# Kernel tuning notes

Measured on AMD Instinct MI355X. Metric: run time of the kernel, lower is better.

The kernel has to match this reference:

```python
import jax, jax.numpy as jnp
import numpy as np

G, N, H, L = 128, 32, 128, 6  # graphs, nodes/graph, hidden, conv layers


def _ln(x, g, b, eps=1e-5):
    m = jnp.mean(x, axis=-1, keepdims=True)
    v = jnp.var(x, axis=-1, keepdims=True)
    return (x - m) * jax.lax.rsqrt(v + eps) * g + b


def setup_inputs() -> dict:
    key = jax.random.key(0)
    ks = jax.random.split(key, 16)
    s = float(H) ** -0.5
    return {
        "x_idx": jax.random.randint(ks[0], (G * N,), 0, 32, dtype=jnp.int32),
        "ea_idx": jax.random.randint(ks[1], (G, N, N), 0, 16, dtype=jnp.int32),
        "tf_idx": jax.random.randint(ks[2], (G, N, N), 0, 16, dtype=jnp.int32),
        "adj": jax.random.randint(ks[3], (G, N, N), 0, 2, dtype=jnp.int32),
        "emb_x": 0.2 * jax.random.normal(ks[4], (32, H), dtype=jnp.float32),
        "emb_ea": 0.2 * jax.random.normal(ks[5], (16, H), dtype=jnp.float32),
        "emb_tf": 0.2 * jax.random.normal(ks[6], (16, H), dtype=jnp.float32),
        "W0": s * jax.random.normal(ks[7], (H, H), dtype=jnp.float32),
        "b0": jnp.zeros((H,), jnp.float32),
        "W1": s * jax.random.normal(ks[8], (H, H), dtype=jnp.float32),
        "b1": jnp.zeros((H,), jnp.float32),
        "Wc": s * jax.random.normal(ks[9], (L, H, H), dtype=jnp.float32),
        "bc": jnp.zeros((L, H), jnp.float32),
        "gc": jnp.ones((L, H), jnp.float32),
        "cc": jnp.zeros((L, H), jnp.float32),
        "Wp": s * jax.random.normal(ks[10], (H, H), dtype=jnp.float32),
        "bp": jnp.zeros((H,), jnp.float32),
        "gp": jnp.ones((H,), jnp.float32),
        "cp": jnp.zeros((H,), jnp.float32),
        "Wq1": s * jax.random.normal(ks[11], (H, H), dtype=jnp.float32),
        "bq1": jnp.zeros((H,), jnp.float32),
        "gq1": jnp.ones((H,), jnp.float32),
        "cq1": jnp.zeros((H,), jnp.float32),
        "Wq2": s * jax.random.normal(ks[12], (H, 1), dtype=jnp.float32),
        "bq2": jnp.zeros((1,), jnp.float32),
    }


def reference(x_idx, ea_idx, tf_idx, adj, emb_x, emb_ea, emb_tf,
              W0, b0, W1, b1, Wc, bc, gc, cc, Wp, bp, gp, cp,
              Wq1, bq1, gq1, cq1, Wq2, bq2):
    # InputEncoderSp: embedding lookups
    x = emb_x[x_idx]                                           # [G*N, H]
    Aval = emb_ea[ea_idx] * adj[..., None].astype(emb_ea.dtype)  # [G,N,N,H] masked edge emb
    # tupleinit: unpooling_fromdense1dim gathers lin(x) to tuple dims 0/1
    x0 = (x @ W0 + b0).reshape(G, N, H)
    x1 = (x @ W1 + b1).reshape(G, N, H)
    X = x0[:, :, None, :] * x1[:, None, :, :] * emb_tf[tf_idx]  # [G,N,N,H]
    for l in range(L):
        tX = jax.nn.relu(_ln(X @ Wc[l] + bc[l], gc[l], cc[l]))
        msg = jnp.einsum('gikh,gkjh->gijh', tX, Aval)          # sum_k tX[i,k]*A[k,j]
        X = X + msg
    # OpPoolingSubg2D('S','mean'): pool tuple dim 1 -> node features
    xs = jnp.mean(X, axis=2).reshape(G * N, H)                 # [G*N, H]
    xs = jax.nn.relu(_ln(xs @ Wp + bp, gp, cp))                # poolmlp
    hg = jnp.sum(xs.reshape(G, N, H), axis=1)                  # node->graph sum pool [G,H]
    # pred_lin: 2-layer MLP, tailact=False
    h = jax.nn.relu(_ln(hg @ Wq1 + bq1, gq1, cq1))
    return h @ Wq2 + bq2                                       # [G, num_tasks=1]
```

## Files before the change

kernel.cpp:

```cpp
#include <hip/hip_runtime.h>

#define G 128
#define N 32
#define H 128
#define L 6

typedef _Float16 half8 __attribute__((ext_vector_type(8)));
typedef float f32x4 __attribute__((ext_vector_type(4)));

union H8 { unsigned u[4]; half8 v; };

__device__ inline unsigned short f16_bits(_Float16 h) {
  union { _Float16 f; unsigned short u; } c; c.f = h; return c.u;
}

__device__ inline unsigned packf16(float x) {
  _Float16 hi = (_Float16)x;
  _Float16 lo = (_Float16)(x - (float)hi);
  return (unsigned)f16_bits(hi) | ((unsigned)f16_bits(lo) << 16);
}

__global__ __launch_bounds__(256) void k_emb_mm(
    const float* __restrict__ emb_x,
    const float* __restrict__ W0, const float* __restrict__ b0, float* __restrict__ P0,
    const float* __restrict__ W1, const float* __restrict__ b1, float* __restrict__ P1) {
  const float* W = blockIdx.x ? W1 : W0;
  const float* b = blockIdx.x ? b1 : b0;
  float*       P = blockIdx.x ? P1 : P0;
  __shared__ float embs_t[128 * 32];
  int tid = threadIdx.x;
  {
    int i = tid & 31, k0 = (tid >> 5) * 16;
    const float* src = emb_x + i * 128 + k0;
#pragma unroll
    for (int m = 0; m < 16; m++) embs_t[(k0 + m) * 32 + i] = src[m];
  }
  __syncthreads();
  int i  = tid >> 3;
  int h0 = (tid & 7) * 16;
  float acc[16];
#pragma unroll
  for (int hh = 0; hh < 16; hh++) acc[hh] = b[h0 + hh];
  for (int k = 0; k < 128; k++) {
    float a = embs_t[k * 32 + i];
    const float4* wr = (const float4*)(W + k * 128 + h0);
    float4 w0 = wr[0], w1 = wr[1], w2 = wr[2], w3 = wr[3];
    acc[0]  += a * w0.x; acc[1]  += a * w0.y; acc[2]  += a * w0.z; acc[3]  += a * w0.w;
    acc[4]  += a * w1.x; acc[5]  += a * w1.y; acc[6]  += a * w1.z; acc[7]  += a * w1.w;
    acc[8]  += a * w2.x; acc[9]  += a * w2.y; acc[10] += a * w2.z; acc[11] += a * w2.w;
    acc[12] += a * w3.x; acc[13] += a * w3.y; acc[14] += a * w3.z; acc[15] += a * w3.w;
  }
  float4* dst = (float4*)(P + i * 128 + h0);
  dst[0] = make_float4(acc[0], acc[1], acc[2], acc[3]);
  dst[1] = make_float4(acc[4], acc[5], acc[6], acc[7]);
  dst[2] = make_float4(acc[8], acc[9], acc[10], acc[11]);
  dst[3] = make_float4(acc[12], acc[13], acc[14], acc[15]);
}

__global__ __launch_bounds__(256) void k_buildX(
    const int* __restrict__ x_idx, const int* __restrict__ tf_idx,
    const float* __restrict__ P0, const float* __restrict__ P1,
    const float* __restrict__ emb_tf, float* __restrict__ Xp) {
  int g = blockIdx.x, tid = threadIdx.x;
  __shared__ float x0t[128 * 32];
  __shared__ float x1t[128 * 32];
  __shared__ float etf[128 * 16];
  __shared__ int   tfs[1024];
  {
    int i = tid & 31, h0 = (tid >> 5) * 16;
    int r = x_idx[g * 32 + i];
    const float* s0 = P0 + r * 128 + h0;
    const float* s1 = P1 + r * 128 + h0;
#pragma unroll
    for (int m = 0; m < 16; m++) {
      x0t[(h0 + m) * 32 + i] = s0[m];
      x1t[(h0 + m) * 32 + i] = s1[m];
    }
  }
  {
    int t = tid & 15, h0 = (tid >> 4) * 8;
    const float* s = emb_tf + t * 128 + h0;
#pragma unroll
    for (int m = 0; m < 8; m++) etf[(h0 + m) * 16 + t] = s[m];
  }
  ((int4*)tfs)[tid] = ((const int4*)(tf_idx + (size_t)g * 1024))[tid];
  __syncthreads();
  int i = tid >> 3, j0 = (tid & 7) * 4;
  int t0 = tfs[i * 32 + j0 + 0], t1 = tfs[i * 32 + j0 + 1];
  int t2 = tfs[i * 32 + j0 + 2], t3 = tfs[i * 32 + j0 + 3];
  float* outg = Xp + ((size_t)g << 17);
  for (int h = 0; h < 128; h++) {
    float a = x0t[h * 32 + i];
    const float* x1r = x1t + h * 32;
    const float* er  = etf + h * 16;
    float4 v;
    v.x = a * x1r[j0 + 0] * er[t0];
    v.y = a * x1r[j0 + 1] * er[t1];
    v.z = a * x1r[j0 + 2] * er[t2];
    v.w = a * x1r[j0 + 3] * er[t3];
    *(float4*)(outg + h * 1024 + tid * 4) = v;
  }
}

__global__ __launch_bounds__(256, 2) void k_conv_mlp(
    const float* __restrict__ Xp, const float* __restrict__ W,
    const float* __restrict__ bcl, const float* __restrict__ gcl,
    const float* __restrict__ ccl, float* __restrict__ tXp) {
  int g = blockIdx.x >> 2, qb = blockIdx.x & 3;
  int tid = threadIdx.x;
  __shared__ unsigned Xs[256 * 32];
  __shared__ unsigned Ws[128 * 32];
  int lane = tid & 63, wv = tid >> 6;
  int x = lane & 15, quad = lane >> 4;

  f32x4 acc[4][8];
#pragma unroll
  for (int hh = 0; hh < 8; hh++) {
    float4 b4 = *(const float4*)(bcl + hh * 16 + quad * 4);
    f32x4 bi; bi[0] = b4.x; bi[1] = b4.y; bi[2] = b4.z; bi[3] = b4.w;
#pragma unroll
    for (int pt = 0; pt < 4; pt++) acc[pt][hh] = bi;
  }

  const float* Xg = Xp + ((size_t)g << 17) + qb * 256;

  for (int c = 0; c < 4; c++) {
    __syncthreads();
    {
      unsigned pk[8][4];
#pragma unroll
      for (int m = 0; m < 8; m++) {
        float4 v = *(const float4*)(Xg + (size_t)(c * 32 + wv * 8 + m) * 1024 + lane * 4);
        pk[m][0] = packf16(v.x); pk[m][1] = packf16(v.y);
        pk[m][2] = packf16(v.z); pk[m][3] = packf16(v.w);
      }
#pragma unroll
      for (int r = 0; r < 4; r++) {
        int p = 4 * lane + r;
        int sw = (p >> 2) & 7;
#pragma unroll
        for (int B2 = 0; B2 < 2; B2++) {
          int B = wv * 2 + B2;
          uint4 q4;
          q4.x = pk[B2 * 4 + 0][r]; q4.y = pk[B2 * 4 + 1][r];
          q4.z = pk[B2 * 4 + 2][r]; q4.w = pk[B2 * 4 + 3][r];
          *(uint4*)&Xs[p * 32 + ((B ^ sw) << 2)] = q4;
        }
      }
    }
    {
#pragma unroll
      for (int m = 0; m < 4; m++) {
        int f4 = m * 64 + lane;
        int kk = wv * 8 + (f4 >> 5);
        int h4 = (f4 & 31) * 4;
        float4 v = *(const float4*)(W + (size_t)(c * 32 + kk) * 128 + h4);
        int Bk = kk >> 2, km = kk & 3;
#pragma unroll
        for (int j = 0; j < 4; j++) {
          float vv = j == 0 ? v.x : (j == 1 ? v.y : (j == 2 ? v.z : v.w));
          int h = h4 + j;
          Ws[h * 32 + (((Bk ^ ((h >> 2) & 7)) << 2) + km)] = packf16(vv);
        }
      }
    }
    __syncthreads();
    H8 bh[4], bl[4];
#pragma unroll
    for (int pt = 0; pt < 4; pt++) {
      int p = wv * 64 + pt * 16 + x;
      int sw = (p >> 2) & 7;
#pragma unroll
      for (int n = 0; n < 4; n++) {
        int k = quad * 8 + n * 2;
        uint2 d = *(const uint2*)&Xs[p * 32 + (((k >> 2) ^ sw) << 2) + (k & 3)];
        bh[pt].u[n] = __builtin_amdgcn_perm(d.y, d.x, 0x05040100u);
        bl[pt].u[n] = __builtin_amdgcn_perm(d.y, d.x, 0x07060302u);
      }
    }
#pragma unroll
    for (int hh = 0; hh < 8; hh++) {
      H8 ah, al;
      int hrow = hh * 16 + x;
      int sw = (hrow >> 2) & 7;
#pragma unroll
      for (int n = 0; n < 4; n++) {
        int k = quad * 8 + n * 2;
        uint2 d = *(const uint2*)&Ws[hrow * 32 + (((k >> 2) ^ sw) << 2) + (k & 3)];
        ah.u[n] = __builtin_amdgcn_perm(d.y, d.x, 0x05040100u);
        al.u[n] = __builtin_amdgcn_perm(d.y, d.x, 0x07060302u);
      }
#pragma unroll
      for (int pt = 0; pt < 4; pt++) {
        acc[pt][hh] = __builtin_amdgcn_mfma_f32_16x16x32_f16(ah.v, bh[pt].v, acc[pt][hh], 0, 0, 0);
        acc[pt][hh] = __builtin_amdgcn_mfma_f32_16x16x32_f16(ah.v, bl[pt].v, acc[pt][hh], 0, 0, 0);
        acc[pt][hh] = __builtin_amdgcn_mfma_f32_16x16x32_f16(al.v, bh[pt].v, acc[pt][hh], 0, 0, 0);
      }
    }
  }

  float gm[4], gr[4];
#pragma unroll
  for (int pt = 0; pt < 4; pt++) {
    float s = 0.f;
#pragma unroll
    for (int hh = 0; hh < 8; hh++)
#pragma unroll
      for (int r = 0; r < 4; r++) s += acc[pt][hh][r];
    s += __shfl_xor(s, 16);
    s += __shfl_xor(s, 32);
    float m = s * (1.f / 128.f);
    float qv = 0.f;
#pragma unroll
    for (int hh = 0; hh < 8; hh++)
#pragma unroll
      for (int r = 0; r < 4; r++) { float d = acc[pt][hh][r] - m; qv += d * d; }
    qv += __shfl_xor(qv, 16);
    qv += __shfl_xor(qv, 32);
    gm[pt] = m;
    gr[pt] = rsqrtf(qv * (1.f / 128.f) + 1e-5f);
  }
  int pbase = qb * 256 + wv * 64;
#pragma unroll
  for (int hh = 0; hh < 8; hh++) {
    float4 g4 = *(const float4*)(gcl + hh * 16 + quad * 4);
    float4 c4 = *(const float4*)(ccl + hh * 16 + quad * 4);
    float ga[4] = {g4.x, g4.y, g4.z, g4.w};
    float ca[4] = {c4.x, c4.y, c4.z, c4.w};
#pragma unroll
    for (int r = 0; r < 4; r++) {
      int h = hh * 16 + quad * 4 + r;
      float* dst = tXp + (((size_t)(g * 128 + h)) << 10) + pbase + x;
#pragma unroll
      for (int pt = 0; pt < 4; pt++) {
        float v = (acc[pt][hh][r] - gm[pt]) * gr[pt] * ga[r] + ca[r];
        dst[pt * 16] = fmaxf(v, 0.f);
      }
    }
  }
}

__global__ __launch_bounds__(256, 4) void k_conv_msg(
    const float* __restrict__ tXp, const int* __restrict__ ea_idx,
    const int* __restrict__ adj, const float* __restrict__ emb_ea,
    float* __restrict__ Xp) {
  int g  = blockIdx.x >> 4;
  int hb = (blockIdx.x & 15) * 8;
  int tid = threadIdx.x, wv = tid >> 6, lane = tid & 63;
  __shared__ unsigned char c8[1024];
  __shared__ float eacs[8][20];
  __shared__ __align__(16) float tXs[4][32 * 36];
  __shared__ __align__(16) float As[4][32 * 36];
  {
    int4 ev = ((const int4*)(ea_idx + (size_t)g * 1024))[tid];
    int4 av = ((const int4*)(adj   + (size_t)g * 1024))[tid];
    uchar4 c;
    c.x = av.x ? (unsigned char)ev.x : (unsigned char)16;
    c.y = av.y ? (unsigned char)ev.y : (unsigned char)16;
    c.z = av.z ? (unsigned char)ev.z : (unsigned char)16;
    c.w = av.w ? (unsigned char)ev.w : (unsigned char)16;
    ((uchar4*)c8)[tid] = c;
  }
  if (tid < 128) {
    int hh = tid >> 4, e = tid & 15;
    eacs[hh][e] = emb_ea[e * 128 + hb + hh];
  }
  if (tid >= 128 && tid < 136) eacs[tid - 128][16] = 0.f;
  __syncthreads();
  int i0 = (lane >> 3) * 4, j0 = (lane & 7) * 4;
  float* tw = tXs[wv];
  float* aw = As[wv];
#pragma unroll 1
  for (int pl = 0; pl < 2; pl++) {
    int hh = wv * 2 + pl;
    int h  = hb + hh;
    const float4* tp = (const float4*)(tXp + (((size_t)(g * 128 + h)) << 10));
#pragma unroll
    for (int m = 0; m < 4; m++) {
      int f = lane + 64 * m;
      float4 v = tp[f];
      *(float4*)&tw[(f >> 3) * 36 + (f & 7) * 4] = v;
    }
#pragma unroll
    for (int m = 0; m < 4; m++) {
      int qd = lane + 64 * m;
      uchar4 cc = ((const uchar4*)c8)[qd];
      float4 a;
      a.x = eacs[hh][cc.x]; a.y = eacs[hh][cc.y];
      a.z = eacs[hh][cc.z]; a.w = eacs[hh][cc.w];
      *(float4*)&aw[(qd >> 3) * 36 + (qd & 7) * 4] = a;
    }
    float4 a0 = {0, 0, 0, 0}, a1 = a0, a2 = a0, a3 = a0;
#pragma unroll
    for (int kb = 0; kb < 8; kb++) {
      int k4 = kb * 4;
      float4 t0 = *(const float4*)&tw[(i0 + 0) * 36 + k4];
      float4 t1 = *(const float4*)&tw[(i0 + 1) * 36 + k4];
      float4 t2 = *(const float4*)&tw[(i0 + 2) * 36 + k4];
      float4 t3 = *(const float4*)&tw[(i0 + 3) * 36 + k4];
      float4 b0 = *(const float4*)&aw[(k4 + 0) * 36 + j0];
      float4 b1 = *(const float4*)&aw[(k4 + 1) * 36 + j0];
      float4 b2 = *(const float4*)&aw[(k4 + 2) * 36 + j0];
      float4 b3 = *(const float4*)&aw[(k4 + 3) * 36 + j0];
      a0.x += t0.x * b0.x; a0.y += t0.x * b0.y; a0.z += t0.x * b0.z; a0.w += t0.x * b0.w;
      a0.x += t0.y * b1.x; a0.y += t0.y * b1.y; a0.z += t0.y * b1.z; a0.w += t0.y * b1.w;
      a0.x += t0.z * b2.x; a0.y += t0.z * b2.y; a0.z += t0.z * b2.z; a0.w += t0.z * b2.w;
      a0.x += t0.w * b3.x; a0.y += t0.w * b3.y; a0.z += t0.w * b3.z; a0.w += t0.w * b3.w;
      a1.x += t1.x * b0.x; a1.y += t1.x * b0.y; a1.z += t1.x * b0.z; a1.w += t1.x * b0.w;
      a1.x += t1.y * b1.x; a1.y += t1.y * b1.y; a1.z += t1.y * b1.z; a1.w += t1.y * b1.w;
      a1.x += t1.z * b2.x; a1.y += t1.z * b2.y; a1.z += t1.z * b2.z; a1.w += t1.z * b2.w;
      a1.x += t1.w * b3.x; a1.y += t1.w * b3.y; a1.z += t1.w * b3.z; a1.w += t1.w * b3.w;
      a2.x += t2.x * b0.x; a2.y += t2.x * b0.y; a2.z += t2.x * b0.z; a2.w += t2.x * b0.w;
      a2.x += t2.y * b1.x; a2.y += t2.y * b1.y; a2.z += t2.y * b1.z; a2.w += t2.y * b1.w;
      a2.x += t2.z * b2.x; a2.y += t2.z * b2.y; a2.z += t2.z * b2.z; a2.w += t2.z * b2.w;
      a2.x += t2.w * b3.x; a2.y += t2.w * b3.y; a2.z += t2.w * b3.z; a2.w += t2.w * b3.w;
      a3.x += t3.x * b0.x; a3.y += t3.x * b0.y; a3.z += t3.x * b0.z; a3.w += t3.x * b0.w;
      a3.x += t3.y * b1.x; a3.y += t3.y * b1.y; a3.z += t3.y * b1.z; a3.w += t3.y * b1.w;
      a3.x += t3.z * b2.x; a3.y += t3.z * b2.y; a3.z += t3.z * b2.z; a3.w += t3.z * b2.w;
      a3.x += t3.w * b3.x; a3.y += t3.w * b3.y; a3.z += t3.w * b3.z; a3.w += t3.w * b3.w;
    }
    float* xr = Xp + (((size_t)(g * 128 + h)) << 10);
    float4* r0 = (float4*)&xr[(i0 + 0) * 32 + j0];
    float4* r1 = (float4*)&xr[(i0 + 1) * 32 + j0];
    float4* r2 = (float4*)&xr[(i0 + 2) * 32 + j0];
    float4* r3 = (float4*)&xr[(i0 + 3) * 32 + j0];
    float4 x0 = *r0, x1 = *r1, x2 = *r2, x3 = *r3;
    x0.x += a0.x; x0.y += a0.y; x0.z += a0.z; x0.w += a0.w;
    x1.x += a1.x; x1.y += a1.y; x1.z += a1.z; x1.w += a1.w;
    x2.x += a2.x; x2.y += a2.y; x2.z += a2.z; x2.w += a2.w;
    x3.x += a3.x; x3.y += a3.y; x3.z += a3.z; x3.w += a3.w;
    *r0 = x0; *r1 = x1; *r2 = x2; *r3 = x3;
  }
}

__global__ __launch_bounds__(256) void k_tail(
    const float* __restrict__ Xp,
    const float* __restrict__ Wp, const float* __restrict__ bp,
    const float* __restrict__ gp, const float* __restrict__ cp,
    const float* __restrict__ Wq1, const float* __restrict__ bq1,
    const float* __restrict__ gq1, const float* __restrict__ cq1,
    const float* __restrict__ Wq2, const float* __restrict__ bq2,
    float* __restrict__ out) {
  int g = blockIdx.x, tid = threadIdx.x;
  __shared__ float xs_s[32 * 132];
  __shared__ float y_s[32 * 132];
  __shared__ float stat_m[32], stat_r[32];
  __shared__ float hg_s[128];
  __shared__ float q_s[128];
  __shared__ float redf[128];
  const float* Xg = Xp + ((size_t)g << 17);
#pragma unroll
  for (int m = 0; m < 16; m++) {
    int rid = m * 256 + tid;
    int hh = rid >> 5, ii = rid & 31;
    const float4* src = (const float4*)(Xg + (size_t)hh * 1024 + ii * 32);
    float s = 0.f;
#pragma unroll
    for (int q = 0; q < 8; q++) { float4 v = src[q]; s += (v.x + v.y) + (v.z + v.w); }
    xs_s[ii * 132 + hh] = s * (1.f / 32.f);
  }
  __syncthreads();
  int i_ = tid >> 3, h0 = (tid & 7) * 16;
  float acc[16];
#pragma unroll
  for (int hh = 0; hh < 16; hh++) acc[hh] = bp[h0 + hh];
  for (int k = 0; k < 128; k++) {
    float a = xs_s[i_ * 132 + k];
    const float4* wr = (const float4*)(Wp + k * 128 + h0);
    float4 w0 = wr[0], w1 = wr[1], w2 = wr[2], w3 = wr[3];
    acc[0]  += a * w0.x; acc[1]  += a * w0.y; acc[2]  += a * w0.z; acc[3]  += a * w0.w;
    acc[4]  += a * w1.x; acc[5]  += a * w1.y; acc[6]  += a * w1.z; acc[7]  += a * w1.w;
    acc[8]  += a * w2.x; acc[9]  += a * w2.y; acc[10] += a * w2.z; acc[11] += a * w2.w;
    acc[12] += a * w3.x; acc[13] += a * w3.y; acc[14] += a * w3.z; acc[15] += a * w3.w;
  }
#pragma unroll
  for (int hh = 0; hh < 16; hh++) y_s[i_ * 132 + h0 + hh] = acc[hh];
  __syncthreads();
  if (tid < 32) {
    float s = 0.f;
    for (int hh = 0; hh < 128; hh++) s += y_s[tid * 132 + hh];
    float m = s * (1.f / 128.f);
    float q = 0.f;
    for (int hh = 0; hh < 128; hh++) { float d = y_s[tid * 132 + hh] - m; q += d * d; }
    stat_m[tid] = m;
    stat_r[tid] = rsqrtf(q * (1.f / 128.f) + 1e-5f);
  }
  __syncthreads();
  {
    float m = stat_m[i_], r = stat_r[i_];
#pragma unroll
    for (int hh = 0; hh < 16; hh++) {
      int hcol = h0 + hh;
      float v = (y_s[i_ * 132 + hcol] - m) * r * gp[hcol] + cp[hcol];
      y_s[i_ * 132 + hcol] = fmaxf(v, 0.f);
    }
  }
  __syncthreads();
  if (tid < 128) {
    float s = 0.f;
#pragma unroll
    for (int ii = 0; ii < 32; ii++) s += y_s[ii * 132 + tid];
    hg_s[tid] = s;
  }
  __syncthreads();
  if (tid < 128) {
    float a = bq1[tid];
    for (int k = 0; k < 128; k++) a += hg_s[k] * Wq1[k * 128 + tid];
    q_s[tid] = a;
  }
  __syncthreads();
  if (tid == 0) {
    float s = 0.f;
    for (int k = 0; k < 128; k++) s += q_s[k];
    float m = s * (1.f / 128.f);
    float q = 0.f;
    for (int k = 0; k < 128; k++) { float d = q_s[k] - m; q += d * d; }
    stat_m[0] = m;
    stat_r[0] = rsqrtf(q * (1.f / 128.f) + 1e-5f);
  }
  __syncthreads();
  if (tid < 128) {
    float v = (q_s[tid] - stat_m[0]) * stat_r[0] * gq1[tid] + cq1[tid];
    v = fmaxf(v, 0.f);
    redf[tid] = v * Wq2[tid];
  }
  __syncthreads();
  if (tid == 0) {
    float s = 0.f;
    for (int k = 0; k < 128; k++) s += redf[k];
    out[g] = s + bq2[0];
  }
}

extern "C" void kernel_launch(void* const* d_in, const int* in_sizes, int n_in,
                              void* d_out, int out_size, void* d_ws, size_t ws_size,
                              hipStream_t stream) {
  const int*   x_idx  = (const int*)d_in[0];
  const int*   ea_idx = (const int*)d_in[1];
  const int*   tf_idx = (const int*)d_in[2];
  const int*   adj    = (const int*)d_in[3];
  const float* emb_x  = (const float*)d_in[4];
  const float* emb_ea = (const float*)d_in[5];
  const float* emb_tf = (const float*)d_in[6];
  const float* W0  = (const float*)d_in[7];
  const float* b0  = (const float*)d_in[8];
  const float* W1  = (const float*)d_in[9];
  const float* b1  = (const float*)d_in[10];
  const float* Wc  = (const float*)d_in[11];
  const float* bc  = (const float*)d_in[12];
  const float* gc  = (const float*)d_in[13];
  const float* cc  = (const float*)d_in[14];
  const float* Wp  = (const float*)d_in[15];
  const float* bp  = (const float*)d_in[16];
  const float* gp  = (const float*)d_in[17];
  const float* cp  = (const float*)d_in[18];
  const float* Wq1 = (const float*)d_in[19];
  const float* bq1 = (const float*)d_in[20];
  const float* gq1 = (const float*)d_in[21];
  const float* cq1 = (const float*)d_in[22];
  const float* Wq2 = (const float*)d_in[23];
  const float* bq2 = (const float*)d_in[24];
  float* out = (float*)d_out;

  float* ws  = (float*)d_ws;
  float* Xp  = ws;
  float* tXp = ws + (size_t)16777216;
  float* P0  = ws + (size_t)33554432;
  float* P1  = P0 + 4096;

  k_emb_mm<<<2, 256, 0, stream>>>(emb_x, W0, b0, P0, W1, b1, P1);
  k_buildX<<<G, 256, 0, stream>>>(x_idx, tf_idx, P0, P1, emb_tf, Xp);
  for (int l = 0; l < L; l++) {
    k_conv_mlp<<<G * 4, 256, 0, stream>>>(Xp, Wc + (size_t)l * H * H,
                                          bc + l * H, gc + l * H, cc + l * H, tXp);
    k_conv_msg<<<G * 16, 256, 0, stream>>>(tXp, ea_idx, adj, emb_ea, Xp);
  }
  k_tail<<<G, 256, 0, stream>>>(Xp, Wp, bp, gp, cp, Wq1, bq1, gq1, cq1, Wq2, bq2, out);
}
```

Measured before the change: 661.4 us.

## Prepack conv weights to fp16 hi/lo, drop LDS staging, fuse mean-pool into last msg

A new pre-kernel splits each conv weight matrix into transposed fp16 hi/lo halves once per call. The MLP kernel then loads its MFMA operands straight from global memory instead of staging them through shared memory with barriers. The last message-passing layer writes mean-pooled node features directly, so the tail kernel no longer rereads the full X tensor, and the tail reductions use wave shuffles. In exchange, the X loads become strided scalar reads with no LDS reuse, and one extra kernel launch is added.

New measurement: 673.1 us. Within noise of the previous version (+1.8%).

```diff
diff --git a/kernel.cpp b/kernel.cpp
--- a/kernel.cpp
+++ b/kernel.cpp
@@ -8,16 +8,19 @@
 typedef _Float16 half8 __attribute__((ext_vector_type(8)));
 typedef float f32x4 __attribute__((ext_vector_type(4)));
 
-union H8 { unsigned u[4]; half8 v; };
-
-__device__ inline unsigned short f16_bits(_Float16 h) {
-  union { _Float16 f; unsigned short u; } c; c.f = h; return c.u;
-}
-
-__device__ inline unsigned packf16(float x) {
-  _Float16 hi = (_Float16)x;
-  _Float16 lo = (_Float16)(x - (float)hi);
-  return (unsigned)f16_bits(hi) | ((unsigned)f16_bits(lo) << 16);
+__global__ __launch_bounds__(256) void k_packW(
+    const float* __restrict__ Wc, _Float16* __restrict__ Wpk) {
+  int l = blockIdx.x, tid = threadIdx.x;
+  const float* W = Wc + (size_t)l * 16384;
+  _Float16* hi = Wpk + (size_t)l * 32768;
+  _Float16* lo = hi + 16384;
+  for (int idx = tid; idx < 16384; idx += 256) {
+    int k = idx >> 7, h = idx & 127;
+    float v = W[idx];
+    _Float16 a = (_Float16)v;
+    hi[h * 128 + k] = a;
+    lo[h * 128 + k] = (_Float16)(v - (float)a);
+  }
 }
 
 __global__ __launch_bounds__(256) void k_emb_mm(
@@ -103,13 +106,11 @@
 }
 
 __global__ __launch_bounds__(256, 2) void k_conv_mlp(
-    const float* __restrict__ Xp, const float* __restrict__ W,
+    const float* __restrict__ Xp, const _Float16* __restrict__ Wpk,
     const float* __restrict__ bcl, const float* __restrict__ gcl,
     const float* __restrict__ ccl, float* __restrict__ tXp) {
   int g = blockIdx.x >> 2, qb = blockIdx.x & 3;
   int tid = threadIdx.x;
-  __shared__ unsigned Xs[256 * 32];
-  __shared__ unsigned Ws[128 * 32];
   int lane = tid & 63, wv = tid >> 6;
   int x = lane & 15, quad = lane >> 4;
 
@@ -122,79 +123,34 @@
     for (int pt = 0; pt < 4; pt++) acc[pt][hh] = bi;
   }
 
-  const float* Xg = Xp + ((size_t)g << 17) + qb * 256;
-
+  const float* Xg = Xp + ((size_t)g << 17) + qb * 256 + wv * 64 + x;
+  const _Float16* Wlo = Wpk + 16384;
+
+#pragma unroll
   for (int c = 0; c < 4; c++) {
-    __syncthreads();
-    {
-      unsigned pk[8][4];
-#pragma unroll
-      for (int m = 0; m < 8; m++) {
-        float4 v = *(const float4*)(Xg + (size_t)(c * 32 + wv * 8 + m) * 1024 + lane * 4);
-        pk[m][0] = packf16(v.x); pk[m][1] = packf16(v.y);
-        pk[m][2] = packf16(v.z); pk[m][3] = packf16(v.w);
+    int kb = c * 32 + quad * 8;
+    half8 bh[4], bl[4];
+#pragma unroll
+    for (int pt = 0; pt < 4; pt++) {
+      const float* xc = Xg + pt * 16 + (size_t)kb * 1024;
+#pragma unroll
+      for (int i = 0; i < 8; i++) {
+        float v = xc[(size_t)i * 1024];
+        _Float16 hi = (_Float16)v;
+        bh[pt][i] = hi;
+        bl[pt][i] = (_Float16)(v - (float)hi);
       }
-#pragma unroll
-      for (int r = 0; r < 4; r++) {
-        int p = 4 * lane + r;
-        int sw = (p >> 2) & 7;
-#pragma unroll
-        for (int B2 = 0; B2 < 2; B2++) {
-          int B = wv * 2 + B2;
-          uint4 q4;
-          q4.x = pk[B2 * 4 + 0][r]; q4.y = pk[B2 * 4 + 1][r];
-          q4.z = pk[B2 * 4 + 2][r]; q4.w = pk[B2 * 4 + 3][r];
-          *(uint4*)&Xs[p * 32 + ((B ^ sw) << 2)] = q4;
-        }
-      }
-    }
-    {
-#pragma unroll
-      for (int m = 0; m < 4; m++) {
-        int f4 = m * 64 + lane;
-        int kk = wv * 8 + (f4 >> 5);
-        int h4 = (f4 & 31) * 4;
-        float4 v = *(const float4*)(W + (size_t)(c * 32 + kk) * 128 + h4);
-        int Bk = kk >> 2, km = kk & 3;
-#pragma unroll
-        for (int j = 0; j < 4; j++) {
-          float vv = j == 0 ? v.x : (j == 1 ? v.y : (j == 2 ? v.z : v.w));
-          int h = h4 + j;
-          Ws[h * 32 + (((Bk ^ ((h >> 2) & 7)) << 2) + km)] = packf16(vv);
-        }
-      }
-    }
-    __syncthreads();
-    H8 bh[4], bl[4];
-#pragma unroll
-    for (int pt = 0; pt < 4; pt++) {
-      int p = wv * 64 + pt * 16 + x;
-      int sw = (p >> 2) & 7;
-#pragma unroll
-      for (int n = 0; n < 4; n++) {
-        int k = quad * 8 + n * 2;
-        uint2 d = *(const uint2*)&Xs[p * 32 + (((k >> 2) ^ sw) << 2) + (k & 3)];
-        bh[pt].u[n] = __builtin_amdgcn_perm(d.y, d.x, 0x05040100u);
-        bl[pt].u[n] = __builtin_amdgcn_perm(d.y, d.x, 0x07060302u);
-      }
     }
 #pragma unroll
     for (int hh = 0; hh < 8; hh++) {
-      H8 ah, al;
-      int hrow = hh * 16 + x;
-      int sw = (hrow >> 2) & 7;
-#pragma unroll
-      for (int n = 0; n < 4; n++) {
-        int k = quad * 8 + n * 2;
-        uint2 d = *(const uint2*)&Ws[hrow * 32 + (((k >> 2) ^ sw) << 2) + (k & 3)];
-        ah.u[n] = __builtin_amdgcn_perm(d.y, d.x, 0x05040100u);
-        al.u[n] = __builtin_amdgcn_perm(d.y, d.x, 0x07060302u);
-      }
+      int wo = (hh * 16 + x) * 128 + kb;
+      half8 ah = *(const half8*)(Wpk + wo);
+      half8 al = *(const half8*)(Wlo + wo);
 #pragma unroll
       for (int pt = 0; pt < 4; pt++) {
-        acc[pt][hh] = __builtin_amdgcn_mfma_f32_16x16x32_f16(ah.v, bh[pt].v, acc[pt][hh], 0, 0, 0);
-        acc[pt][hh] = __builtin_amdgcn_mfma_f32_16x16x32_f16(ah.v, bl[pt].v, acc[pt][hh], 0, 0, 0);
-        acc[pt][hh] = __builtin_amdgcn_mfma_f32_16x16x32_f16(al.v, bh[pt].v, acc[pt][hh], 0, 0, 0);
+        acc[pt][hh] = __builtin_amdgcn_mfma_f32_16x16x32_f16(ah, bh[pt], acc[pt][hh], 0, 0, 0);
+        acc[pt][hh] = __builtin_amdgcn_mfma_f32_16x16x32_f16(ah, bl[pt], acc[pt][hh], 0, 0, 0);
+        acc[pt][hh] = __builtin_amdgcn_mfma_f32_16x16x32_f16(al, bh[pt], acc[pt][hh], 0, 0, 0);
       }
     }
   }
@@ -240,10 +196,11 @@
   }
 }
 
+template <bool LAST>
 __global__ __launch_bounds__(256, 4) void k_conv_msg(
     const float* __restrict__ tXp, const int* __restrict__ ea_idx,
     const int* __restrict__ adj, const float* __restrict__ emb_ea,
-    float* __restrict__ Xp) {
+    float* __restrict__ Xp, float* __restrict__ xs) {
   int g  = blockIdx.x >> 4;
   int hb = (blockIdx.x & 15) * 8;
   int tid = threadIdx.x, wv = tid >> 6, lane = tid & 63;
@@ -329,12 +286,30 @@
     x1.x += a1.x; x1.y += a1.y; x1.z += a1.z; x1.w += a1.w;
     x2.x += a2.x; x2.y += a2.y; x2.z += a2.z; x2.w += a2.w;
     x3.x += a3.x; x3.y += a3.y; x3.z += a3.z; x3.w += a3.w;
-    *r0 = x0; *r1 = x1; *r2 = x2; *r3 = x3;
-  }
-}
-
-__global__ __launch_bounds__(256) void k_tail(
-    const float* __restrict__ Xp,
+    if (!LAST) {
+      *r0 = x0; *r1 = x1; *r2 = x2; *r3 = x3;
+    } else {
+      float s0 = (x0.x + x0.y) + (x0.z + x0.w);
+      float s1 = (x1.x + x1.y) + (x1.z + x1.w);
+      float s2 = (x2.x + x2.y) + (x2.z + x2.w);
+      float s3 = (x3.x + x3.y) + (x3.z + x3.w);
+      s0 += __shfl_xor(s0, 1); s0 += __shfl_xor(s0, 2); s0 += __shfl_xor(s0, 4);
+      s1 += __shfl_xor(s1, 1); s1 += __shfl_xor(s1, 2); s1 += __shfl_xor(s1, 4);
+      s2 += __shfl_xor(s2, 1); s2 += __shfl_xor(s2, 2); s2 += __shfl_xor(s2, 4);
+      s3 += __shfl_xor(s3, 1); s3 += __shfl_xor(s3, 2); s3 += __shfl_xor(s3, 4);
+      if ((lane & 7) == 0) {
+        float* xo = xs + ((size_t)(g * 32 + i0)) * 128 + h;
+        xo[0]   = s0 * (1.f / 32.f);
+        xo[128] = s1 * (1.f / 32.f);
+        xo[256] = s2 * (1.f / 32.f);
+        xo[384] = s3 * (1.f / 32.f);
+      }
+    }
+  }
+}
+
+__global__ __launch_bounds__(256) void k_tail2(
+    const float* __restrict__ xs,
     const float* __restrict__ Wp, const float* __restrict__ bp,
     const float* __restrict__ gp, const float* __restrict__ cp,
     const float* __restrict__ Wq1, const float* __restrict__ bq1,
@@ -342,30 +317,28 @@
     const float* __restrict__ Wq2, const float* __restrict__ bq2,
     float* __restrict__ out) {
   int g = blockIdx.x, tid = threadIdx.x;
-  __shared__ float xs_s[32 * 132];
+  __shared__ float xsl[32 * 132];
   __shared__ float y_s[32 * 132];
-  __shared__ float stat_m[32], stat_r[32];
+  __shared__ float red8[32][9];
   __shared__ float hg_s[128];
   __shared__ float q_s[128];
-  __shared__ float redf[128];
-  const float* Xg = Xp + ((size_t)g << 17);
-#pragma unroll
-  for (int m = 0; m < 16; m++) {
-    int rid = m * 256 + tid;
-    int hh = rid >> 5, ii = rid & 31;
-    const float4* src = (const float4*)(Xg + (size_t)hh * 1024 + ii * 32);
-    float s = 0.f;
-#pragma unroll
-    for (int q = 0; q < 8; q++) { float4 v = src[q]; s += (v.x + v.y) + (v.z + v.w); }
-    xs_s[ii * 132 + hh] = s * (1.f / 32.f);
-  }
-  __syncthreads();
-  int i_ = tid >> 3, h0 = (tid & 7) * 16;
+  __shared__ float stat[2];
+  {
+    const float4* src = (const float4*)(xs + (size_t)g * 4096);
+#pragma unroll
+    for (int m = 0; m < 4; m++) {
+      int f = m * 256 + tid;
+      int row = f >> 5, col = (f & 31) * 4;
+      *(float4*)&xsl[row * 132 + col] = src[f];
+    }
+  }
+  __syncthreads();
+  int i_ = tid >> 3, ht = tid & 7, h0 = ht * 16;
   float acc[16];
 #pragma unroll
   for (int hh = 0; hh < 16; hh++) acc[hh] = bp[h0 + hh];
   for (int k = 0; k < 128; k++) {
-    float a = xs_s[i_ * 132 + k];
+    float a = xsl[i_ * 132 + k];
     const float4* wr = (const float4*)(Wp + k * 128 + h0);
     float4 w0 = wr[0], w1 = wr[1], w2 = wr[2], w3 = wr[3];
     acc[0]  += a * w0.x; acc[1]  += a * w0.y; acc[2]  += a * w0.z; acc[3]  += a * w0.w;
@@ -373,34 +346,40 @@
     acc[8]  += a * w2.x; acc[9]  += a * w2.y; acc[10] += a * w2.z; acc[11] += a * w2.w;
     acc[12] += a * w3.x; acc[13] += a * w3.y; acc[14] += a * w3.z; acc[15] += a * w3.w;
   }
-#pragma unroll
-  for (int hh = 0; hh < 16; hh++) y_s[i_ * 132 + h0 + hh] = acc[hh];
-  __syncthreads();
-  if (tid < 32) {
+  {
     float s = 0.f;
-    for (int hh = 0; hh < 128; hh++) s += y_s[tid * 132 + hh];
-    float m = s * (1.f / 128.f);
+#pragma unroll
+    for (int hh = 0; hh < 16; hh++) s += acc[hh];
+    red8[i_][ht] = s;
+  }
+  __syncthreads();
+  float m = 0.f;
+#pragma unroll
+  for (int t = 0; t < 8; t++) m += red8[i_][t];
+  m *= (1.f / 128.f);
+  __syncthreads();
+  {
     float q = 0.f;
-    for (int hh = 0; hh < 128; hh++) { float d = y_s[tid * 132 + hh] - m; q += d * d; }
-    stat_m[tid] = m;
-    stat_r[tid] = rsqrtf(q * (1.f / 128.f) + 1e-5f);
-  }
-  __syncthreads();
-  {
-    float m = stat_m[i_], r = stat_r[i_];
-#pragma unroll
-    for (int hh = 0; hh < 16; hh++) {
-      int hcol = h0 + hh;
-      float v = (y_s[i_ * 132 + hcol] - m) * r * gp[hcol] + cp[hcol];
-      y_s[i_ * 132 + hcol] = fmaxf(v, 0.f);
-    }
+#pragma unroll
+    for (int hh = 0; hh < 16; hh++) { float d = acc[hh] - m; q += d * d; }
+    red8[i_][ht] = q;
+  }
+  __syncthreads();
+  float v = 0.f;
+#pragma unroll
+  for (int t = 0; t < 8; t++) v += red8[i_][t];
+  float r = rsqrtf(v * (1.f / 128.f) + 1e-5f);
+#pragma unroll
+  for (int hh = 0; hh < 16; hh++) {
+    int hcol = h0 + hh;
+    y_s[i_ * 132 + hcol] = fmaxf((acc[hh] - m) * r * gp[hcol] + cp[hcol], 0.f);
   }
   __syncthreads();
   if (tid < 128) {
-    float s = 0.f;
-#pragma unroll
-    for (int ii = 0; ii < 32; ii++) s += y_s[ii * 132 + tid];
-    hg_s[tid] = s;
+    float sh = 0.f;
+#pragma unroll
+    for (int ii = 0; ii < 32; ii++) sh += y_s[ii * 132 + tid];
+    hg_s[tid] = sh;
   }
   __syncthreads();
   if (tid < 128) {
@@ -409,26 +388,30 @@
     q_s[tid] = a;
   }
   __syncthreads();
-  if (tid == 0) {
-    float s = 0.f;
-    for (int k = 0; k < 128; k++) s += q_s[k];
-    float m = s * (1.f / 128.f);
-    float q = 0.f;
-    for (int k = 0; k < 128; k++) { float d = q_s[k] - m; q += d * d; }
-    stat_m[0] = m;
-    stat_r[0] = rsqrtf(q * (1.f / 128.f) + 1e-5f);
-  }
-  __syncthreads();
-  if (tid < 128) {
-    float v = (q_s[tid] - stat_m[0]) * stat_r[0] * gq1[tid] + cq1[tid];
-    v = fmaxf(v, 0.f);
-    redf[tid] = v * Wq2[tid];
-  }
-  __syncthreads();
-  if (tid == 0) {
-    float s = 0.f;
-    for (int k = 0; k < 128; k++) s += redf[k];
-    out[g] = s + bq2[0];
+  if (tid < 64) {
+    float s2 = q_s[tid] + q_s[tid + 64];
+    s2 += __shfl_xor(s2, 1);  s2 += __shfl_xor(s2, 2);  s2 += __shfl_xor(s2, 4);
+    s2 += __shfl_xor(s2, 8);  s2 += __shfl_xor(s2, 16); s2 += __shfl_xor(s2, 32);
+    if (tid == 0) stat[0] = s2 * (1.f / 128.f);
+  }
+  __syncthreads();
+  float mq = stat[0];
+  if (tid < 64) {
+    float d0 = q_s[tid] - mq, d1 = q_s[tid + 64] - mq;
+    float v2 = d0 * d0 + d1 * d1;
+    v2 += __shfl_xor(v2, 1);  v2 += __shfl_xor(v2, 2);  v2 += __shfl_xor(v2, 4);
+    v2 += __shfl_xor(v2, 8);  v2 += __shfl_xor(v2, 16); v2 += __shfl_xor(v2, 32);
+    if (tid == 0) stat[1] = rsqrtf(v2 * (1.f / 128.f) + 1e-5f);
+  }
+  __syncthreads();
+  float rq = stat[1];
+  if (tid < 64) {
+    float a0 = fmaxf((q_s[tid]      - mq) * rq * gq1[tid]      + cq1[tid],      0.f) * Wq2[tid];
+    float a1 = fmaxf((q_s[tid + 64] - mq) * rq * gq1[tid + 64] + cq1[tid + 64], 0.f) * Wq2[tid + 64];
+    float t = a0 + a1;
+    t += __shfl_xor(t, 1);  t += __shfl_xor(t, 2);  t += __shfl_xor(t, 4);
+    t += __shfl_xor(t, 8);  t += __shfl_xor(t, 16); t += __shfl_xor(t, 32);
+    if (tid == 0) out[g] = t + bq2[0];
   }
 }
 
@@ -467,13 +450,19 @@
   float* tXp = ws + (size_t)16777216;
   float* P0  = ws + (size_t)33554432;
   float* P1  = P0 + 4096;
-
+  float* xs  = ws + (size_t)33562624;
+  _Float16* Wpk = (_Float16*)(ws + (size_t)34086912);
+
+  k_packW<<<6, 256, 0, stream>>>(Wc, Wpk);
   k_emb_mm<<<2, 256, 0, stream>>>(emb_x, W0, b0, P0, W1, b1, P1);
   k_buildX<<<G, 256, 0, stream>>>(x_idx, tf_idx, P0, P1, emb_tf, Xp);
   for (int l = 0; l < L; l++) {
-    k_conv_mlp<<<G * 4, 256, 0, stream>>>(Xp, Wc + (size_t)l * H * H,
+    k_conv_mlp<<<G * 4, 256, 0, stream>>>(Xp, Wpk + (size_t)l * 32768,
                                           bc + l * H, gc + l * H, cc + l * H, tXp);
-    k_conv_msg<<<G * 16, 256, 0, stream>>>(tXp, ea_idx, adj, emb_ea, Xp);
-  }
-  k_tail<<<G, 256, 0, stream>>>(Xp, Wp, bp, gp, cp, Wq1, bq1, gq1, cq1, Wq2, bq2, out);
-}
+    if (l < L - 1)
+      k_conv_msg<false><<<G * 16, 256, 0, stream>>>(tXp, ea_idx, adj, emb_ea, Xp, xs);
+    else
+      k_conv_msg<true><<<G * 16, 256, 0, stream>>>(tXp, ea_idx, adj, emb_ea, Xp, xs);
+  }
+  k_tail2<<<G, 256, 0, stream>>>(xs, Wp, bp, gp, cp, Wq1, bq1, gq1, cq1, Wq2, bq2, out);
+}
```
